# Kernel tuning notes

Measured on AMD Instinct MI355X. Metric: run time of the kernel, lower is better.

Reference implementation:

```python
import jax, jax.numpy as jnp
import numpy as np

H = 20  # hidden size (hard-coded in the module)

def setup_inputs() -> dict:
    key = jax.random.key(0)
    ks = jax.random.split(key, 7)
    B, T = 4096, 1000
    s = 1.0 / np.sqrt(H)  # torch default init bound for RNN/Linear
    x = jax.random.normal(ks[0], (B, T, 1), dtype=jnp.float32)
    W_ih = jax.random.uniform(ks[1], (H, 1), jnp.float32, -s, s)
    W_hh = jax.random.uniform(ks[2], (H, H), jnp.float32, -s, s)
    b_ih = jax.random.uniform(ks[3], (H,), jnp.float32, -s, s)
    b_hh = jax.random.uniform(ks[4], (H,), jnp.float32, -s, s)
    fc_w = jax.random.uniform(ks[5], (1, H), jnp.float32, -s, s)
    fc_b = jax.random.uniform(ks[6], (1,), jnp.float32, -s, s)
    return {"x": x, "W_ih": W_ih, "W_hh": W_hh, "b_ih": b_ih,
            "b_hh": b_hh, "fc_w": fc_w, "fc_b": fc_b}

def reference(x, W_ih, W_hh, b_ih, b_hh, fc_w, fc_b):
    # x: [B, T, 1] -> time-major [T, B, 1] for scan
    B = x.shape[0]
    xt = jnp.swapaxes(x, 0, 1)
    # precompute input projection for all timesteps: [T, B, H]
    xproj = jnp.einsum('tbi,hi->tbh', xt, W_ih) + b_ih + b_hh
    h0 = jnp.zeros((B, H), dtype=x.dtype)
    def step(h, xp_t):
        h_new = jax.nn.relu(xp_t + h @ W_hh.T)
        return h_new, None
    h_last, _ = jax.lax.scan(step, h0, xproj)
    # only the last hidden state feeds the head: fc1(rnn_out[:, -1, :])
    out = h_last @ fc_w.T + fc_b  # [B, 1]
    return out
```

## Files before the change

### kernel.cpp

```cpp
#include <hip/hip_runtime.h>


#define TT 1000

typedef float v2f __attribute__((ext_vector_type(2)));

struct Col { v2f p01, p23; float v4; };

#define PIN(v)  asm volatile("" : "+v"(v))
__device__ __forceinline__ void pinc(Col& c) {
    PIN(c.p01); PIN(c.p23); PIN(c.v4);
}
__device__ __forceinline__ void keepc(const Col& c) {
    asm volatile("" :: "v"(c.p01), "v"(c.p23), "v"(c.v4));
}

template <int CTRL>
__device__ __forceinline__ float dpp_f(float v) {
    return __int_as_float(__builtin_amdgcn_update_dpp(
        0, __float_as_int(v), CTRL, 0xF, 0xF, true));
}

#define QP_XOR1 0xB1
#define QP_XOR2 0x4E
#define ROR4   0x124
#define ROR8   0x128

template <int HALF, int C1, int C2>
__device__ __forceinline__ void step(v2f xp, v2f& h01, v2f& h23, float& h4,
                                     const Col& wc0, const Col& wc1,
                                     const Col& wc2, const Col& wc3,
                                     const Col& wc4,
                                     const Col& wih, const Col& bias) {
    const v2f xs = (HALF == 0) ? xp.xx : xp.yy;
    const float xt = (HALF == 0) ? xp.x : xp.y;

    v2f  X01 = __builtin_elementwise_fma(xs, wih.p01, bias.p01);
    v2f  X23 = __builtin_elementwise_fma(xs, wih.p23, bias.p23);
    float x4 = __builtin_fmaf(xt, wih.v4, bias.v4);

    X01 = __builtin_elementwise_fma(h01.xx, wc0.p01, X01);
    X23 = __builtin_elementwise_fma(h01.xx, wc0.p23, X23);
    x4  = __builtin_fmaf(h01.x, wc0.v4, x4);
    X01 = __builtin_elementwise_fma(h01.yy, wc1.p01, X01);
    X23 = __builtin_elementwise_fma(h01.yy, wc1.p23, X23);
    x4  = __builtin_fmaf(h01.y, wc1.v4, x4);

    v2f  Y01 = h23.xx * wc2.p01;
    v2f  Y23 = h23.xx * wc2.p23;
    float y4 = h23.x * wc2.v4;

    Y01 = __builtin_elementwise_fma(h23.yy, wc3.p01, Y01);
    Y23 = __builtin_elementwise_fma(h23.yy, wc3.p23, Y23);
    y4  = __builtin_fmaf(h23.y, wc3.v4, y4);
    { const v2f h4s = {h4, h4};
      Y01 = __builtin_elementwise_fma(h4s, wc4.p01, Y01);
      Y23 = __builtin_elementwise_fma(h4s, wc4.p23, Y23);
      y4  = __builtin_fmaf(h4, wc4.v4, y4); }

    v2f  A01 = X01 + Y01;
    v2f  A23 = X23 + Y23;
    float a4 = x4 + y4;

    float b0 = A01.x, b1 = A01.y, b2 = A23.x, b3 = A23.y, b4 = a4;
    {
        float t0 = dpp_f<C1>(b0), t1 = dpp_f<C1>(b1), t2 = dpp_f<C1>(b2),
              t3 = dpp_f<C1>(b3), t4 = dpp_f<C1>(b4);
        b0 += t0; b1 += t1; b2 += t2; b3 += t3; b4 += t4;
    }
    {
        float t0 = dpp_f<C2>(b0), t1 = dpp_f<C2>(b1), t2 = dpp_f<C2>(b2),
              t3 = dpp_f<C2>(b3), t4 = dpp_f<C2>(b4);
        b0 += t0; b1 += t1; b2 += t2; b3 += t3; b4 += t4;
    }

    const v2f z = {0.f, 0.f};
    v2f r01 = {b0, b1};
    v2f r23 = {b2, b3};
    h01 = __builtin_elementwise_max(r01, z);
    h23 = __builtin_elementwise_max(r23, z);
    h4  = fmaxf(b4, 0.f);
}

__global__ void
__attribute__((amdgpu_flat_work_group_size(64, 64), amdgpu_waves_per_eu(1, 1)))
rnn_os_kernel(const float* __restrict__ x,
              const float* __restrict__ W_ih,
              const float* __restrict__ W_hh,
              const float* __restrict__ b_ih,
              const float* __restrict__ b_hh,
              const float* __restrict__ fc_w,
              const float* __restrict__ fc_b,
              float* __restrict__ out) {
    const int tid = blockIdx.x * 64 + threadIdx.x;
    const int b   = tid >> 4;
    const int gl  = tid & 15;
    const int a   = gl >> 2;
    const int bq  = gl & 3;

    Col we0, we1, we2, we3, we4;
    Col wo0, wo1, wo2, wo3, wo4;
#define LOADC(wk, k, rbase, cbase)                                            \
    { (wk).p01 = (v2f){ W_hh[((rbase) + 0) * 20 + (cbase) + (k)],             \
                        W_hh[((rbase) + 1) * 20 + (cbase) + (k)] };           \
      (wk).p23 = (v2f){ W_hh[((rbase) + 2) * 20 + (cbase) + (k)],             \
                        W_hh[((rbase) + 3) * 20 + (cbase) + (k)] };           \
      (wk).v4  =        W_hh[((rbase) + 4) * 20 + (cbase) + (k)]; }
    LOADC(we0, 0, a * 5, bq * 5) LOADC(we1, 1, a * 5, bq * 5)
    LOADC(we2, 2, a * 5, bq * 5) LOADC(we3, 3, a * 5, bq * 5)
    LOADC(we4, 4, a * 5, bq * 5)
    LOADC(wo0, 0, bq * 5, a * 5) LOADC(wo1, 1, bq * 5, a * 5)
    LOADC(wo2, 2, bq * 5, a * 5) LOADC(wo3, 3, bq * 5, a * 5)
    LOADC(wo4, 4, bq * 5, a * 5)
#undef LOADC

    const bool eact = (bq == 0);
    const bool oact = (a == 0);
    Col wie, bie, wio, bio;
#define LOADIB(wv, bv, base, act)                                             \
    { const float* pw = W_ih + (base);                                        \
      const float* p1 = b_ih + (base);                                        \
      const float* p2 = b_hh + (base);                                        \
      (wv).p01 = (v2f){ (act) ? pw[0] : 0.f, (act) ? pw[1] : 0.f };           \
      (wv).p23 = (v2f){ (act) ? pw[2] : 0.f, (act) ? pw[3] : 0.f };           \
      (wv).v4  =        (act) ? pw[4] : 0.f;                                  \
      (bv).p01 = (v2f){ (act) ? (p1[0] + p2[0]) : 0.f,                        \
                        (act) ? (p1[1] + p2[1]) : 0.f };                      \
      (bv).p23 = (v2f){ (act) ? (p1[2] + p2[2]) : 0.f,                        \
                        (act) ? (p1[3] + p2[3]) : 0.f };                      \
      (bv).v4  =        (act) ? (p1[4] + p2[4]) : 0.f; }
    LOADIB(wie, bie, a * 5,  eact)
    LOADIB(wio, bio, bq * 5, oact)
#undef LOADIB

    pinc(we0); pinc(we1); pinc(we2); pinc(we3); pinc(we4);
    pinc(wo0); pinc(wo1); pinc(wo2); pinc(wo3); pinc(wo4);
    pinc(wie); pinc(bie); pinc(wio); pinc(bio);

    v2f h01 = {0.f, 0.f}, h23 = {0.f, 0.f};
    float h4 = 0.f;

    const float* __restrict__ xb = x + (size_t)b * TT;

#define LOAD5(P, off)                                   \
    P##0 = *(const float4*)(xb + (off));                \
    P##1 = *(const float4*)(xb + (off) + 4);            \
    P##2 = *(const float4*)(xb + (off) + 8);            \
    P##3 = *(const float4*)(xb + (off) + 12);           \
    P##4 = *(const float4*)(xb + (off) + 16);

#define STEP_E(xp, H) step<H, QP_XOR1, QP_XOR2>(xp, h01, h23, h4, we0, we1, we2, we3, we4, wie, bie);
#define STEP_O(xp, H) step<H, ROR4,    ROR8   >(xp, h01, h23, h4, wo0, wo1, wo2, wo3, wo4, wio, bio);
#define RUN4(Q) {                                       \
        const v2f qlo = {Q.x, Q.y};                     \
        const v2f qhi = {Q.z, Q.w};                     \
        STEP_E(qlo, 0) STEP_O(qlo, 1)                   \
        STEP_E(qhi, 0) STEP_O(qhi, 1) }
#define RUN20(P) RUN4(P##0) RUN4(P##1) RUN4(P##2) RUN4(P##3) RUN4(P##4)

    float4 A0, A1, A2, A3, A4;
    float4 B0, B1, B2, B3, B4;
    LOAD5(A, 0)
    LOAD5(B, 20)

    for (int it = 0; it < 24; ++it) {
        const int base = it * 40;
        RUN20(A)
        LOAD5(A, base + 40)
        RUN20(B)
        LOAD5(B, base + 60)
    }
    RUN20(A)
    RUN20(B)

#undef RUN20
#undef RUN4
#undef STEP_E
#undef STEP_O
#undef LOAD5

    keepc(we0); keepc(we1); keepc(we2); keepc(we3); keepc(we4);
    keepc(wo0); keepc(wo1); keepc(wo2); keepc(wo3); keepc(wo4);
    keepc(wie); keepc(bie); keepc(wio); keepc(bio);

    float dot;
    {
        const float* pf = fc_w + bq * 5;
        float f0 = oact ? pf[0] : 0.f, f1 = oact ? pf[1] : 0.f;
        float f2 = oact ? pf[2] : 0.f, f3 = oact ? pf[3] : 0.f;
        float f4 = oact ? pf[4] : 0.f;
        dot = h01.x * f0;
        dot = __builtin_fmaf(h01.y, f1, dot);
        dot = __builtin_fmaf(h23.x, f2, dot);
        dot = __builtin_fmaf(h23.y, f3, dot);
        dot = __builtin_fmaf(h4,    f4, dot);
    }
    dot += __shfl_xor(dot, 1, 16);
    dot += __shfl_xor(dot, 2, 16);
    dot += __shfl_xor(dot, 4, 16);
    dot += __shfl_xor(dot, 8, 16);

    if (gl == 0)
        out[b] = dot + fc_b[0];
}

extern "C" void kernel_launch(void* const* d_in, const int* in_sizes, int n_in,
                              void* d_out, int out_size, void* d_ws, size_t ws_size,
                              hipStream_t stream) {
    const float* x    = (const float*)d_in[0];
    const float* W_ih = (const float*)d_in[1];
    const float* W_hh = (const float*)d_in[2];
    const float* b_ih = (const float*)d_in[3];
    const float* b_hh = (const float*)d_in[4];
    const float* fc_w = (const float*)d_in[5];
    const float* fc_b = (const float*)d_in[6];
    float* out = (float*)d_out;

    const int block = 64;
    const int grid  = (4096 * 16) / block;
    rnn_os_kernel<<<grid, block, 0, stream>>>(x, W_ih, W_hh, b_ih, b_hh,
                                              fc_w, fc_b, out);
}
```

Measured before the change: 152.9 us.

## Split each batch row across 4 lanes with quad-rotate DPP gathers

```diff
diff --git a/kernel.cpp b/kernel.cpp
--- a/kernel.cpp
+++ b/kernel.cpp
@@ -15,71 +15,14 @@
     asm volatile("" :: "v"(c.p01), "v"(c.p23), "v"(c.v4));
 }
 
+#define QP_ROR1 0x39
+#define QP_ROR2 0x4E
+#define QP_ROR3 0x93
+
 template <int CTRL>
-__device__ __forceinline__ float dpp_f(float v) {
+__device__ __forceinline__ float dpp_mov(float v) {
     return __int_as_float(__builtin_amdgcn_update_dpp(
         0, __float_as_int(v), CTRL, 0xF, 0xF, true));
-}
-
-#define QP_XOR1 0xB1
-#define QP_XOR2 0x4E
-#define ROR4   0x124
-#define ROR8   0x128
-
-template <int HALF, int C1, int C2>
-__device__ __forceinline__ void step(v2f xp, v2f& h01, v2f& h23, float& h4,
-                                     const Col& wc0, const Col& wc1,
-                                     const Col& wc2, const Col& wc3,
-                                     const Col& wc4,
-                                     const Col& wih, const Col& bias) {
-    const v2f xs = (HALF == 0) ? xp.xx : xp.yy;
-    const float xt = (HALF == 0) ? xp.x : xp.y;
-
-    v2f  X01 = __builtin_elementwise_fma(xs, wih.p01, bias.p01);
-    v2f  X23 = __builtin_elementwise_fma(xs, wih.p23, bias.p23);
-    float x4 = __builtin_fmaf(xt, wih.v4, bias.v4);
-
-    X01 = __builtin_elementwise_fma(h01.xx, wc0.p01, X01);
-    X23 = __builtin_elementwise_fma(h01.xx, wc0.p23, X23);
-    x4  = __builtin_fmaf(h01.x, wc0.v4, x4);
-    X01 = __builtin_elementwise_fma(h01.yy, wc1.p01, X01);
-    X23 = __builtin_elementwise_fma(h01.yy, wc1.p23, X23);
-    x4  = __builtin_fmaf(h01.y, wc1.v4, x4);
-
-    v2f  Y01 = h23.xx * wc2.p01;
-    v2f  Y23 = h23.xx * wc2.p23;
-    float y4 = h23.x * wc2.v4;
-
-    Y01 = __builtin_elementwise_fma(h23.yy, wc3.p01, Y01);
-    Y23 = __builtin_elementwise_fma(h23.yy, wc3.p23, Y23);
-    y4  = __builtin_fmaf(h23.y, wc3.v4, y4);
-    { const v2f h4s = {h4, h4};
-      Y01 = __builtin_elementwise_fma(h4s, wc4.p01, Y01);
-      Y23 = __builtin_elementwise_fma(h4s, wc4.p23, Y23);
-      y4  = __builtin_fmaf(h4, wc4.v4, y4); }
-
-    v2f  A01 = X01 + Y01;
-    v2f  A23 = X23 + Y23;
-    float a4 = x4 + y4;
-
-    float b0 = A01.x, b1 = A01.y, b2 = A23.x, b3 = A23.y, b4 = a4;
-    {
-        float t0 = dpp_f<C1>(b0), t1 = dpp_f<C1>(b1), t2 = dpp_f<C1>(b2),
-              t3 = dpp_f<C1>(b3), t4 = dpp_f<C1>(b4);
-        b0 += t0; b1 += t1; b2 += t2; b3 += t3; b4 += t4;
-    }
-    {
-        float t0 = dpp_f<C2>(b0), t1 = dpp_f<C2>(b1), t2 = dpp_f<C2>(b2),
-              t3 = dpp_f<C2>(b3), t4 = dpp_f<C2>(b4);
-        b0 += t0; b1 += t1; b2 += t2; b3 += t3; b4 += t4;
-    }
-
-    const v2f z = {0.f, 0.f};
-    v2f r01 = {b0, b1};
-    v2f r23 = {b2, b3};
-    h01 = __builtin_elementwise_max(r01, z);
-    h23 = __builtin_elementwise_max(r23, z);
-    h4  = fmaxf(b4, 0.f);
 }
 
 __global__ void
@@ -93,54 +36,105 @@
               const float* __restrict__ fc_b,
               float* __restrict__ out) {
     const int tid = blockIdx.x * 64 + threadIdx.x;
-    const int b   = tid >> 4;
-    const int gl  = tid & 15;
-    const int a   = gl >> 2;
-    const int bq  = gl & 3;
-
-    Col we0, we1, we2, we3, we4;
-    Col wo0, wo1, wo2, wo3, wo4;
-#define LOADC(wk, k, rbase, cbase)                                            \
-    { (wk).p01 = (v2f){ W_hh[((rbase) + 0) * 20 + (cbase) + (k)],             \
-                        W_hh[((rbase) + 1) * 20 + (cbase) + (k)] };           \
-      (wk).p23 = (v2f){ W_hh[((rbase) + 2) * 20 + (cbase) + (k)],             \
-                        W_hh[((rbase) + 3) * 20 + (cbase) + (k)] };           \
-      (wk).v4  =        W_hh[((rbase) + 4) * 20 + (cbase) + (k)]; }
-    LOADC(we0, 0, a * 5, bq * 5) LOADC(we1, 1, a * 5, bq * 5)
-    LOADC(we2, 2, a * 5, bq * 5) LOADC(we3, 3, a * 5, bq * 5)
-    LOADC(we4, 4, a * 5, bq * 5)
-    LOADC(wo0, 0, bq * 5, a * 5) LOADC(wo1, 1, bq * 5, a * 5)
-    LOADC(wo2, 2, bq * 5, a * 5) LOADC(wo3, 3, bq * 5, a * 5)
-    LOADC(wo4, 4, bq * 5, a * 5)
-#undef LOADC
-
-    const bool eact = (bq == 0);
-    const bool oact = (a == 0);
-    Col wie, bie, wio, bio;
-#define LOADIB(wv, bv, base, act)                                             \
-    { const float* pw = W_ih + (base);                                        \
-      const float* p1 = b_ih + (base);                                        \
-      const float* p2 = b_hh + (base);                                        \
-      (wv).p01 = (v2f){ (act) ? pw[0] : 0.f, (act) ? pw[1] : 0.f };           \
-      (wv).p23 = (v2f){ (act) ? pw[2] : 0.f, (act) ? pw[3] : 0.f };           \
-      (wv).v4  =        (act) ? pw[4] : 0.f;                                  \
-      (bv).p01 = (v2f){ (act) ? (p1[0] + p2[0]) : 0.f,                        \
-                        (act) ? (p1[1] + p2[1]) : 0.f };                      \
-      (bv).p23 = (v2f){ (act) ? (p1[2] + p2[2]) : 0.f,                        \
-                        (act) ? (p1[3] + p2[3]) : 0.f };                      \
-      (bv).v4  =        (act) ? (p1[4] + p2[4]) : 0.f; }
-    LOADIB(wie, bie, a * 5,  eact)
-    LOADIB(wio, bio, bq * 5, oact)
-#undef LOADIB
-
-    pinc(we0); pinc(we1); pinc(we2); pinc(we3); pinc(we4);
-    pinc(wo0); pinc(wo1); pinc(wo2); pinc(wo3); pinc(wo4);
-    pinc(wie); pinc(bie); pinc(wio); pinc(bio);
+    const int b   = tid >> 2;
+    const int j   = tid & 3;
+
+    Col c0, c1, c2, c3, c4, c5, c6, c7, c8, c9,
+        c10, c11, c12, c13, c14, c15, c16, c17, c18, c19;
+#define LOADS(ck, s)                                                          \
+    { const int own = (j + (s) / 5) & 3;                                      \
+      const int ci  = own * 5 + (s) % 5;                                      \
+      (ck).p01 = (v2f){ W_hh[(j * 5 + 0) * 20 + ci],                          \
+                        W_hh[(j * 5 + 1) * 20 + ci] };                        \
+      (ck).p23 = (v2f){ W_hh[(j * 5 + 2) * 20 + ci],                          \
+                        W_hh[(j * 5 + 3) * 20 + ci] };                        \
+      (ck).v4  =        W_hh[(j * 5 + 4) * 20 + ci]; }
+    LOADS(c0, 0)   LOADS(c1, 1)   LOADS(c2, 2)   LOADS(c3, 3)   LOADS(c4, 4)
+    LOADS(c5, 5)   LOADS(c6, 6)   LOADS(c7, 7)   LOADS(c8, 8)   LOADS(c9, 9)
+    LOADS(c10, 10) LOADS(c11, 11) LOADS(c12, 12) LOADS(c13, 13) LOADS(c14, 14)
+    LOADS(c15, 15) LOADS(c16, 16) LOADS(c17, 17) LOADS(c18, 18) LOADS(c19, 19)
+#undef LOADS
+
+    Col wie, bie;
+    {
+        const float* pw = W_ih + j * 5;
+        const float* p1 = b_ih + j * 5;
+        const float* p2 = b_hh + j * 5;
+        wie.p01 = (v2f){ pw[0], pw[1] };
+        wie.p23 = (v2f){ pw[2], pw[3] };
+        wie.v4  = pw[4];
+        bie.p01 = (v2f){ p1[0] + p2[0], p1[1] + p2[1] };
+        bie.p23 = (v2f){ p1[2] + p2[2], p1[3] + p2[3] };
+        bie.v4  = p1[4] + p2[4];
+    }
+
+    pinc(c0); pinc(c1); pinc(c2); pinc(c3); pinc(c4);
+    pinc(c5); pinc(c6); pinc(c7); pinc(c8); pinc(c9);
+    pinc(c10); pinc(c11); pinc(c12); pinc(c13); pinc(c14);
+    pinc(c15); pinc(c16); pinc(c17); pinc(c18); pinc(c19);
+    pinc(wie); pinc(bie);
 
     v2f h01 = {0.f, 0.f}, h23 = {0.f, 0.f};
     float h4 = 0.f;
 
     const float* __restrict__ xb = x + (size_t)b * TT;
+
+    auto step1 = [&](float xt) {
+        v2f g101, g123; float g14;
+        v2f g201, g223; float g24;
+        v2f g301, g323; float g34;
+        g101.x = dpp_mov<QP_ROR1>(h01.x); g101.y = dpp_mov<QP_ROR1>(h01.y);
+        g123.x = dpp_mov<QP_ROR1>(h23.x); g123.y = dpp_mov<QP_ROR1>(h23.y);
+        g14    = dpp_mov<QP_ROR1>(h4);
+        g201.x = dpp_mov<QP_ROR2>(h01.x); g201.y = dpp_mov<QP_ROR2>(h01.y);
+        g223.x = dpp_mov<QP_ROR2>(h23.x); g223.y = dpp_mov<QP_ROR2>(h23.y);
+        g24    = dpp_mov<QP_ROR2>(h4);
+        g301.x = dpp_mov<QP_ROR3>(h01.x); g301.y = dpp_mov<QP_ROR3>(h01.y);
+        g323.x = dpp_mov<QP_ROR3>(h23.x); g323.y = dpp_mov<QP_ROR3>(h23.y);
+        g34    = dpp_mov<QP_ROR3>(h4);
+
+#define MACC(A01, A23, a4, hs, hk, ck)                                  \
+        A01 = __builtin_elementwise_fma(hs, (ck).p01, A01);             \
+        A23 = __builtin_elementwise_fma(hs, (ck).p23, A23);             \
+        a4  = __builtin_fmaf(hk, (ck).v4, a4);
+
+        const v2f xs = {xt, xt};
+        v2f  X01 = __builtin_elementwise_fma(xs, wie.p01, bie.p01);
+        v2f  X23 = __builtin_elementwise_fma(xs, wie.p23, bie.p23);
+        float x4 = __builtin_fmaf(xt, wie.v4, bie.v4);
+        MACC(X01, X23, x4, h01.xx, h01.x, c0)
+        MACC(X01, X23, x4, h01.yy, h01.y, c1)
+        MACC(X01, X23, x4, h23.xx, h23.x, c2)
+        MACC(X01, X23, x4, h23.yy, h23.y, c3)
+        { const v2f s = {h4, h4};   MACC(X01, X23, x4, s, h4, c4) }
+        MACC(X01, X23, x4, g101.xx, g101.x, c5)
+        MACC(X01, X23, x4, g101.yy, g101.y, c6)
+        MACC(X01, X23, x4, g123.xx, g123.x, c7)
+        MACC(X01, X23, x4, g123.yy, g123.y, c8)
+        { const v2f s = {g14, g14}; MACC(X01, X23, x4, s, g14, c9) }
+
+        v2f  Y01 = g201.xx * c10.p01;
+        v2f  Y23 = g201.xx * c10.p23;
+        float y4 = g201.x  * c10.v4;
+        MACC(Y01, Y23, y4, g201.yy, g201.y, c11)
+        MACC(Y01, Y23, y4, g223.xx, g223.x, c12)
+        MACC(Y01, Y23, y4, g223.yy, g223.y, c13)
+        { const v2f s = {g24, g24}; MACC(Y01, Y23, y4, s, g24, c14) }
+        MACC(Y01, Y23, y4, g301.xx, g301.x, c15)
+        MACC(Y01, Y23, y4, g301.yy, g301.y, c16)
+        MACC(Y01, Y23, y4, g323.xx, g323.x, c17)
+        MACC(Y01, Y23, y4, g323.yy, g323.y, c18)
+        { const v2f s = {g34, g34}; MACC(Y01, Y23, y4, s, g34, c19) }
+#undef MACC
+
+        const v2f z = {0.f, 0.f};
+        v2f A01 = X01 + Y01;
+        v2f A23 = X23 + Y23;
+        float a4 = x4 + y4;
+        h01 = __builtin_elementwise_max(A01, z);
+        h23 = __builtin_elementwise_max(A23, z);
+        h4  = fmaxf(a4, 0.f);
+    };
 
 #define LOAD5(P, off)                                   \
     P##0 = *(const float4*)(xb + (off));                \
@@ -149,13 +143,7 @@
     P##3 = *(const float4*)(xb + (off) + 12);           \
     P##4 = *(const float4*)(xb + (off) + 16);
 
-#define STEP_E(xp, H) step<H, QP_XOR1, QP_XOR2>(xp, h01, h23, h4, we0, we1, we2, we3, we4, wie, bie);
-#define STEP_O(xp, H) step<H, ROR4,    ROR8   >(xp, h01, h23, h4, wo0, wo1, wo2, wo3, wo4, wio, bio);
-#define RUN4(Q) {                                       \
-        const v2f qlo = {Q.x, Q.y};                     \
-        const v2f qhi = {Q.z, Q.w};                     \
-        STEP_E(qlo, 0) STEP_O(qlo, 1)                   \
-        STEP_E(qhi, 0) STEP_O(qhi, 1) }
+#define RUN4(Q) { step1(Q.x); step1(Q.y); step1(Q.z); step1(Q.w); }
 #define RUN20(P) RUN4(P##0) RUN4(P##1) RUN4(P##2) RUN4(P##3) RUN4(P##4)
 
     float4 A0, A1, A2, A3, A4;
@@ -175,32 +163,27 @@
 
 #undef RUN20
 #undef RUN4
-#undef STEP_E
-#undef STEP_O
 #undef LOAD5
 
-    keepc(we0); keepc(we1); keepc(we2); keepc(we3); keepc(we4);
-    keepc(wo0); keepc(wo1); keepc(wo2); keepc(wo3); keepc(wo4);
-    keepc(wie); keepc(bie); keepc(wio); keepc(bio);
+    keepc(c0); keepc(c1); keepc(c2); keepc(c3); keepc(c4);
+    keepc(c5); keepc(c6); keepc(c7); keepc(c8); keepc(c9);
+    keepc(c10); keepc(c11); keepc(c12); keepc(c13); keepc(c14);
+    keepc(c15); keepc(c16); keepc(c17); keepc(c18); keepc(c19);
+    keepc(wie); keepc(bie);
 
     float dot;
     {
-        const float* pf = fc_w + bq * 5;
-        float f0 = oact ? pf[0] : 0.f, f1 = oact ? pf[1] : 0.f;
-        float f2 = oact ? pf[2] : 0.f, f3 = oact ? pf[3] : 0.f;
-        float f4 = oact ? pf[4] : 0.f;
-        dot = h01.x * f0;
-        dot = __builtin_fmaf(h01.y, f1, dot);
-        dot = __builtin_fmaf(h23.x, f2, dot);
-        dot = __builtin_fmaf(h23.y, f3, dot);
-        dot = __builtin_fmaf(h4,    f4, dot);
+        const float* pf = fc_w + j * 5;
+        dot = h01.x * pf[0];
+        dot = __builtin_fmaf(h01.y, pf[1], dot);
+        dot = __builtin_fmaf(h23.x, pf[2], dot);
+        dot = __builtin_fmaf(h23.y, pf[3], dot);
+        dot = __builtin_fmaf(h4,    pf[4], dot);
     }
-    dot += __shfl_xor(dot, 1, 16);
-    dot += __shfl_xor(dot, 2, 16);
-    dot += __shfl_xor(dot, 4, 16);
-    dot += __shfl_xor(dot, 8, 16);
-
-    if (gl == 0)
+    dot += __shfl_xor(dot, 1, 4);
+    dot += __shfl_xor(dot, 2, 4);
+
+    if (j == 0)
         out[b] = dot + fc_b[0];
 }
 
@@ -217,7 +200,7 @@
     float* out = (float*)d_out;
 
     const int block = 64;
-    const int grid  = (4096 * 16) / block;
+    const int grid  = (4096 * 4) / block;
     rnn_os_kernel<<<grid, block, 0, stream>>>(x, W_ih, W_hh, b_ih, b_hh,
                                               fc_w, fc_b, out);
 }
```

Result: slower. 233.3 us (+52.6%).
